# Kernel optimization log

Measured on AMD Instinct MI355X. Metric: run time of the kernel, lower is better.

The kernel has to match this reference:

```python
import jax, jax.numpy as jnp
import numpy as np

EPS = 1e-5

def _bn_train(x, gamma, beta):
    # BatchNorm2d in training mode: batch stats over (N,H,W), biased variance
    mean = jnp.mean(x, axis=(0, 2, 3), keepdims=True)
    var = jnp.mean((x - mean) ** 2, axis=(0, 2, 3), keepdims=True)
    xn = (x - mean) / jnp.sqrt(var + EPS)
    return xn * gamma[None, :, None, None] + beta[None, :, None, None]

def _bin_act(x):
    # forward: sign(x); backward: grad of clamp(x,-1,1) (STE)
    c = jnp.clip(x, -1.0, 1.0)
    return jax.lax.stop_gradient(jnp.sign(x) - c) + c

def _bin_conv(x, w_flat, out_chn, in_chn, k=3, stride=1, padding=1):
    w = w_flat.reshape(out_chn, in_chn, k, k)
    scale = jax.lax.stop_gradient(jnp.mean(jnp.abs(w), axis=(1, 2, 3), keepdims=True))
    cw = jnp.clip(w, -1.0, 1.0)
    bw = jax.lax.stop_gradient(scale * jnp.sign(w) - cw) + cw
    return jax.lax.conv_general_dilated(
        x, bw, window_strides=(stride, stride),
        padding=[(padding, padding), (padding, padding)],
        dimension_numbers=('NCHW', 'OIHW', 'NCHW'))

def _prelu(x, a):
    return jnp.where(x >= 0, x, a * x)

def setup_inputs() -> dict:
    key = jax.random.key(0)
    ks = jax.random.split(key, 4)
    C = 128
    x = jax.random.normal(ks[0], (64, C, 56, 56), dtype=jnp.float32)
    # HardBinaryConv stores weights as (n,1); init small, mixed-sign
    w1 = (jax.random.uniform(ks[1], (C * C * 9, 1), dtype=jnp.float32) - 0.5) * 0.002
    w2 = (jax.random.uniform(ks[2], (C * C * 9, 1), dtype=jnp.float32) - 0.5) * 0.002
    ones = jnp.ones((C,), jnp.float32)
    zeros = jnp.zeros((C,), jnp.float32)
    a = jnp.float32(0.25)
    return {
        'x': x,
        'bn1_g': ones, 'bn1_b': zeros,
        'w1': w1, 'prelu1_a': a,
        'bn2_g': ones, 'bn2_b': zeros,
        'w2': w2, 'prelu2_a': a,
        'bn3_g': ones, 'bn3_b': zeros,
        'prelu3_a': a,
    }

def reference(x, bn1_g, bn1_b, w1, prelu1_a, bn2_g, bn2_b, w2, prelu2_a, bn3_g, bn3_b, prelu3_a):
    C = x.shape[1]
    out = _bn_train(x, bn1_g, bn1_b)
    out = _bin_act(out)
    out = _prelu(_bin_conv(out, w1, C, C), prelu1_a)
    out = _bn_train(out, bn2_g, bn2_b)
    out = _bin_act(out)
    out = _bin_conv(out, w2, C, C)
    out = _prelu(out, prelu2_a)
    out = _bn_train(out, bn3_g, bn3_b)
    out = out + x  # identity shortcut (stride=1, in_planes==planes)
    out = _prelu(out, prelu3_a)
    return out
```

## Files before the change

### kernel.cpp

```cpp
#include <hip/hip_runtime.h>
#include <hip/hip_bf16.h>

typedef __attribute__((ext_vector_type(8))) short short8;
typedef __attribute__((ext_vector_type(4))) int i32x4;

#define HW     3136
#define M_TOT  200704
#define NTAP   9
#define NBLK   896
#define SLABB  44544

__device__ __forceinline__ void gload_lds16(const void* g, void* l) {
    __builtin_amdgcn_global_load_lds(
        (const __attribute__((address_space(1))) void*)g,
        (__attribute__((address_space(3))) void*)l, 16, 0, 0);
}

__global__ __launch_bounds__(256) void wprep_kernel(const float* __restrict__ w1,
                                                    const float* __restrict__ w2,
                                                    float* __restrict__ scale1,
                                                    float* __restrict__ scale2,
                                                    char* __restrict__ ws1,
                                                    char* __restrict__ ws2) {
    int t = threadIdx.x;
    if (blockIdx.x < 256) {
        int o = blockIdx.x;
        const float* w = w1;
        float* scale = scale1;
        if (o >= 128) { o -= 128; w = w2; scale = scale2; }
        float s = 0.f;
        for (int i = t; i < 1152; i += 256) s += fabsf(w[o * 1152 + i]);
        __shared__ float r1[256];
        r1[t] = s; __syncthreads();
        for (int off = 128; off > 0; off >>= 1) {
            if (t < off) r1[t] += r1[t + off];
            __syncthreads();
        }
        if (t == 0) scale[o] = r1[0] * (1.f / 1152.f);
        return;
    }
    int i = (blockIdx.x - 256) * 256 + t;
    const float* w = w1;
    char* wsz = ws1;
    if (i >= 147456) { i -= 147456; w = w2; wsz = ws2; }
    int e = i & 15, l = (i >> 4) & 63, f = (i >> 10) & 7, s = i >> 13;
    int cout = f * 16 + (l & 15);
    int k = s * 64 + (l >> 4) * 16 + e;
    int tap = k >> 7, cin = k & 127;
    float v = w[(cout * 128 + cin) * 9 + tap];
    wsz[i] = v > 0.f ? (char)1 : (v < 0.f ? (char)-1 : (char)0);
}

__global__ __launch_bounds__(256) void stats_nchw_kernel(const float* __restrict__ x,
                                                         float* __restrict__ psum,
                                                         float* __restrict__ psq) {
    int bid = blockIdx.x;
    int n = bid >> 7, c = bid & 127;
    const float* p = x + (n * 128 + c) * HW;
    int t = threadIdx.x;
    float s = 0.f, q = 0.f;
    for (int i4 = t; i4 < 784; i4 += 256) {
        float4 v = *(const float4*)(p + i4 * 4);
        s += v.x + v.y + v.z + v.w;
        q += v.x * v.x + v.y * v.y + v.z * v.z + v.w * v.w;
    }
    __shared__ float r1[256], r2[256];
    r1[t] = s; r2[t] = q; __syncthreads();
    for (int off = 128; off > 0; off >>= 1) {
        if (t < off) { r1[t] += r1[t + off]; r2[t] += r2[t + off]; }
        __syncthreads();
    }
    if (t == 0) { psum[c * 64 + n] = r1[0]; psq[c * 64 + n] = r2[0]; }
}

__global__ __launch_bounds__(256) void finalizeB_kernel(const float* __restrict__ psumB,
                                                        const float* __restrict__ psqB,
                                                        float* __restrict__ mean,
                                                        float* __restrict__ rstd) {
    int c = blockIdx.x, t = threadIdx.x;
    float s = 0.f, q = 0.f;
    for (int j = t; j < NBLK; j += 256) { s += psumB[j * 128 + c]; q += psqB[j * 128 + c]; }
    __shared__ float r1[256], r2[256];
    r1[t] = s; r2[t] = q; __syncthreads();
    for (int off = 128; off > 0; off >>= 1) {
        if (t < off) { r1[t] += r1[t + off]; r2[t] += r2[t + off]; }
        __syncthreads();
    }
    if (t == 0) {
        const float invN = 1.f / 200704.f;
        float m = r1[0] * invN;
        float var = r2[0] * invN - m * m;
        mean[c] = m;
        rstd[c] = 1.f / sqrtf(var + 1e-5f);
    }
}

__global__ __launch_bounds__(256) void act1_kernel(const float* __restrict__ x,
        const float* __restrict__ psum, const float* __restrict__ psq,
        const float* __restrict__ g, const float* __restrict__ b,
        char* __restrict__ apad) {
    __shared__ float row[128 * 57];
    __shared__ float smean[128], srstd[128];
    int blk = blockIdx.x;
    int n = blk / 58, hp = blk - n * 58;
    char* o = apad + (n * 58 + hp) * 58 * 128;
    int t = threadIdx.x;
    if (hp == 0 || hp == 57) {
        for (int i4 = t; i4 < 58 * 32; i4 += 256)
            *(char4*)(o + i4 * 4) = make_char4(0, 0, 0, 0);
        return;
    }
    if (t < 128) {
        float s = 0.f, q = 0.f;
        for (int j = 0; j < 64; ++j) { s += psum[t * 64 + j]; q += psq[t * 64 + j]; }
        const float invN = 1.f / 200704.f;
        float m = s * invN;
        float var = q * invN - m * m;
        smean[t] = m;
        srstd[t] = 1.f / sqrtf(var + 1e-5f);
    }
    const float* src = x + n * (128 * HW) + (hp - 1) * 56;
    for (int i4 = t; i4 < 128 * 14; i4 += 256) {
        int c = i4 / 14, w4 = (i4 - c * 14) * 4;
        float4 v = *(const float4*)(src + c * HW + w4);
        row[c * 57 + w4 + 0] = v.x;
        row[c * 57 + w4 + 1] = v.y;
        row[c * 57 + w4 + 2] = v.z;
        row[c * 57 + w4 + 3] = v.w;
    }
    __syncthreads();
    for (int i4 = t; i4 < 58 * 32; i4 += 256) {
        int wp = i4 >> 5;
        int c0 = (i4 & 31) * 4;
        char q[4] = {0, 0, 0, 0};
        if (wp >= 1 && wp <= 56) {
#pragma unroll
            for (int k = 0; k < 4; ++k) {
                int c = c0 + k;
                float xn = (row[c * 57 + wp - 1] - smean[c]) * srstd[c] * g[c] + b[c];
                q[k] = xn > 0.f ? 1 : (xn < 0.f ? -1 : 0);
            }
        }
        *(char4*)(o + wp * 128 + c0) = make_char4(q[0], q[1], q[2], q[3]);
    }
}

__global__ __launch_bounds__(256) void act2_kernel(const short* __restrict__ p1,
        const float* __restrict__ scale1, const float* __restrict__ a1ptr,
        const float* __restrict__ mean, const float* __restrict__ rstd,
        const float* __restrict__ g, const float* __restrict__ b,
        char* __restrict__ apad) {
    __shared__ float row[128 * 57];
    int blk = blockIdx.x;
    int n = blk / 58, hp = blk - n * 58;
    char* o = apad + (n * 58 + hp) * 58 * 128;
    int t = threadIdx.x;
    if (hp == 0 || hp == 57) {
        for (int i4 = t; i4 < 58 * 32; i4 += 256)
            *(char4*)(o + i4 * 4) = make_char4(0, 0, 0, 0);
        return;
    }
    float a1 = a1ptr[0];
    const short* src = p1 + n * HW + (hp - 1) * 56;
    for (int i8 = t; i8 < 128 * 7; i8 += 256) {
        int c = i8 / 7, w8 = (i8 - c * 7) * 8;
        short8 v = *(const short8*)(src + (size_t)c * M_TOT + w8);
        float sc = scale1[c];
#pragma unroll
        for (int k = 0; k < 8; ++k) {
            float val = sc * (float)v[k];
            row[c * 57 + w8 + k] = val >= 0.f ? val : a1 * val;
        }
    }
    __syncthreads();
    for (int i4 = t; i4 < 58 * 32; i4 += 256) {
        int wp = i4 >> 5;
        int c0 = (i4 & 31) * 4;
        char q[4] = {0, 0, 0, 0};
        if (wp >= 1 && wp <= 56) {
#pragma unroll
            for (int k = 0; k < 4; ++k) {
                int c = c0 + k;
                float xn = (row[c * 57 + wp - 1] - mean[c]) * rstd[c] * g[c] + b[c];
                q[k] = xn > 0.f ? 1 : (xn < 0.f ? -1 : 0);
            }
        }
        *(char4*)(o + wp * 128 + c0) = make_char4(q[0], q[1], q[2], q[3]);
    }
}

template<bool RAW, typename OutT>
__global__ __launch_bounds__(256, 2) void conv_kernel(
        const char* __restrict__ apad,
        const char* __restrict__ wswz,
        const float* __restrict__ scale,
        const float* __restrict__ aptr,
        OutT* __restrict__ obuf,
        float* __restrict__ psumB,
        float* __restrict__ psqB) {
    __shared__ __align__(1024) char lds[SLABB + 2 * 16384];

    const int tid = threadIdx.x;
    const int lane = tid & 63;
    const int wid = tid >> 6;
    const int l15 = lane & 15;
    const int lq = lane >> 4;
    const int wr = wid >> 1;
    const int wc = wid & 1;

    int bid = blockIdx.x;
    int mblk = (bid & 7) * 112 + (bid >> 3);
    const int n = mblk / 14;
    const int hg = mblk - n * 14;
    const int m0 = n * HW + hg * 224;

    const char* slabsrc = apad + (size_t)(n * 58 + hg * 4) * 58 * 128;
    char* slab = lds;
    char* Abuf = lds + SLABB;

    {
#pragma unroll
        for (int i = 0; i < 11; ++i) {
            int gbyte = i * 4096 + tid * 16;
            if (i < 10 || gbyte < SLABB) {
                int r = gbyte >> 7;
                int cp = (gbyte >> 4) & 7;
                int wp = r % 58;
                gload_lds16(slabsrc + (gbyte & ~127) + ((cp ^ (wp & 7)) << 4),
                            slab + i * 4096 + wid * 1024);
            }
        }
    }

    int Pm[7], Wm[7];
#pragma unroll
    for (int mi = 0; mi < 7; ++mi) {
        int mloc = wc * 112 + mi * 16 + l15;
        int ho = mloc / 56;
        int w = mloc - ho * 56;
        Pm[mi] = (ho * 58 + w) * 128;
        Wm[mi] = w;
    }

    auto stageA = [&](int t, int buf) {
        const char* wsrc = wswz + t * 16384 + tid * 16;
        char* dst = Abuf + buf * 16384 + wid * 1024;
#pragma unroll
        for (int i = 0; i < 4; ++i)
            gload_lds16(wsrc + i * 4096, dst + i * 4096);
    };

    i32x4 acc[4][7];
#pragma unroll
    for (int i = 0; i < 4; ++i)
#pragma unroll
        for (int j = 0; j < 7; ++j)
            acc[i][j] = (i32x4){0, 0, 0, 0};

    stageA(0, 0);

    for (int t = 0; t < NTAP; ++t) {
        asm volatile("s_waitcnt vmcnt(0)" ::: "memory");
        __builtin_amdgcn_s_barrier();
        if (t + 1 < NTAP) stageA(t + 1, (t + 1) & 1);

        int dh = t / 3;
        int dw = t - dh * 3;
        int Q = (dh * 58 + dw) * 128;
        const char* abuf = Abuf + (t & 1) * 16384;

#pragma unroll
        for (int ks = 0; ks < 2; ++ks) {
            i32x4 af[4], bf[7];
#pragma unroll
            for (int ci = 0; ci < 4; ++ci)
                af[ci] = *(const i32x4*)(abuf + ks * 8192 + (wr * 4 + ci) * 1024 + lane * 16);
            int c16 = ks * 4 + lq;
#pragma unroll
            for (int mi = 0; mi < 7; ++mi) {
                int wxd = (Wm[mi] + dw) & 7;
                bf[mi] = *(const i32x4*)(slab + Pm[mi] + Q + ((c16 ^ wxd) << 4));
            }
            __builtin_amdgcn_s_setprio(1);
#pragma unroll
            for (int ci = 0; ci < 4; ++ci)
#pragma unroll
                for (int mi = 0; mi < 7; ++mi)
                    acc[ci][mi] = __builtin_amdgcn_mfma_i32_16x16x64_i8(
                        af[ci], bf[mi], acc[ci][mi], 0, 0, 0);
            __builtin_amdgcn_s_setprio(0);
        }
    }

    float alpha = aptr[0];
    float* partS = (float*)(Abuf + 16384);
    float* partQ = (float*)(Abuf + 16384 + 1024);
#pragma unroll
    for (int ci = 0; ci < 4; ++ci) {
        int cb = wr * 64 + ci * 16 + lq * 4;
#pragma unroll
        for (int r = 0; r < 4; ++r) {
            float sc = scale[cb + r];
            OutT* op = obuf + (size_t)(cb + r) * M_TOT + m0 + wc * 112 + l15;
            float s = 0.f, q = 0.f;
#pragma unroll
            for (int mi = 0; mi < 7; ++mi) {
                int iv = acc[ci][mi][r];
                float v = (float)iv * sc;
                float pv = v >= 0.f ? v : alpha * v;
                if constexpr (RAW) op[mi * 16] = (OutT)(short)iv;
                else               op[mi * 16] = (OutT)__float2bfloat16(pv);
                s += pv; q += pv * pv;
            }
#pragma unroll
            for (int msk = 1; msk <= 8; msk <<= 1) {
                s += __shfl_xor(s, msk, 64);
                q += __shfl_xor(q, msk, 64);
            }
            if (l15 == 0) { partS[wc * 128 + cb + r] = s; partQ[wc * 128 + cb + r] = q; }
        }
    }
    __syncthreads();
    if (tid < 128) {
        psumB[bid * 128 + tid] = partS[tid] + partS[128 + tid];
        psqB [bid * 128 + tid] = partQ[tid] + partQ[128 + tid];
    }
}

__global__ __launch_bounds__(256) void final_kernel(const __hip_bfloat16* __restrict__ p2,
        const float* __restrict__ x,
        const float* __restrict__ mean, const float* __restrict__ rstd,
        const float* __restrict__ g, const float* __restrict__ b,
        const float* __restrict__ a3ptr, float* __restrict__ out) {
    int bid = blockIdx.x;
    int n = bid >> 7, c = bid & 127;
    float m = mean[c], r = rstd[c], gg = g[c], bb = b[c], a3 = a3ptr[0];
    const __hip_bfloat16* pp = p2 + (size_t)c * M_TOT + n * HW;
    const float* xx = x + (n * 128 + c) * HW;
    float* oo = out + (n * 128 + c) * HW;
    int t = threadIdx.x;
    for (int i8 = t; i8 < 392; i8 += 256) {
        short8 v = *(const short8*)(pp + i8 * 8);
        float4 x0 = *(const float4*)(xx + i8 * 8);
        float4 x1 = *(const float4*)(xx + i8 * 8 + 4);
        float o[8];
#pragma unroll
        for (int k = 0; k < 8; ++k) {
            float pv = __uint_as_float(((unsigned int)(unsigned short)v[k]) << 16);
            float xv = (k < 4) ? ((const float*)&x0)[k] : ((const float*)&x1)[k - 4];
            float val = (pv - m) * r * gg + bb + xv;
            o[k] = val >= 0.f ? val : a3 * val;
        }
        *(float4*)(oo + i8 * 8)     = make_float4(o[0], o[1], o[2], o[3]);
        *(float4*)(oo + i8 * 8 + 4) = make_float4(o[4], o[5], o[6], o[7]);
    }
}

extern "C" void kernel_launch(void* const* d_in, const int* in_sizes, int n_in,
                              void* d_out, int out_size, void* d_ws, size_t ws_size,
                              hipStream_t stream) {
    const float* x  = (const float*)d_in[0];
    const float* g1 = (const float*)d_in[1];
    const float* b1 = (const float*)d_in[2];
    const float* w1 = (const float*)d_in[3];
    const float* a1 = (const float*)d_in[4];
    const float* g2 = (const float*)d_in[5];
    const float* b2 = (const float*)d_in[6];
    const float* w2 = (const float*)d_in[7];
    const float* a2 = (const float*)d_in[8];
    const float* g3 = (const float*)d_in[9];
    const float* b3 = (const float*)d_in[10];
    const float* a3 = (const float*)d_in[11];
    float* out = (float*)d_out;
    char* ws = (char*)d_ws;

    float* scale1 = (float*)(ws);
    float* scale2 = (float*)(ws + 512);
    float* mean2  = (float*)(ws + 2048);
    float* rstd2  = (float*)(ws + 2560);
    float* mean3  = (float*)(ws + 3072);
    float* rstd3  = (float*)(ws + 3584);
    float* psum   = (float*)(ws + 4096);
    float* psq    = (float*)(ws + 36864);
    float* psumB  = (float*)(ws + 69632);
    float* psqB   = (float*)(ws + 872448);
    char* wswz1   = (char*)(ws + 1675264);
    char* wswz2   = (char*)(ws + 1822720);
    char* apad8   = (char*)(ws + 1970176);
    __hip_bfloat16* buf2b = (__hip_bfloat16*)(ws + 29528064);
    short* buf1s  = (short*)out;

    wprep_kernel<<<1408, 256, 0, stream>>>(w1, w2, scale1, scale2, wswz1, wswz2);

    stats_nchw_kernel<<<8192, 256, 0, stream>>>(x, psum, psq);
    act1_kernel<<<3712, 256, 0, stream>>>(x, psum, psq, g1, b1, apad8);
    conv_kernel<true, short><<<NBLK, 256, 0, stream>>>(apad8, wswz1, scale1, a1,
                                                       buf1s, psumB, psqB);

    finalizeB_kernel<<<128, 256, 0, stream>>>(psumB, psqB, mean2, rstd2);
    act2_kernel<<<3712, 256, 0, stream>>>(buf1s, scale1, a1, mean2, rstd2, g2, b2, apad8);
    conv_kernel<false, __hip_bfloat16><<<NBLK, 256, 0, stream>>>(apad8, wswz2, scale2, a2,
                                                                 buf2b, psumB, psqB);

    finalizeB_kernel<<<128, 256, 0, stream>>>(psumB, psqB, mean3, rstd3);
    final_kernel<<<8192, 256, 0, stream>>>(buf2b, x, mean3, rstd3, g3, b3, a3, out);
}
```

Baseline: 242.7 us.

## Shrink weight LDS staging to single half-tap buffer for 3 blocks/CU

Removes the double-buffered 16KB-per-tap weight staging and instead loads an 8KB half-tap chunk each of 18 steps into a single buffer. The smaller LDS footprint (about 54KB instead of 76KB) and launch bounds raised to 3 blocks per CU aim to increase occupancy. The cost is that weight loads are no longer prefetched: each step waits on its own global load and adds a second barrier, so latency hiding now depends on the extra resident blocks. Accumulator register pressure under the tighter launch bound may also cause spills.

```diff
diff --git a/kernel.cpp b/kernel.cpp
--- a/kernel.cpp
+++ b/kernel.cpp
@@ -6,7 +6,7 @@
 
 #define HW     3136
 #define M_TOT  200704
-#define NTAP   9
+#define NSTEP  18
 #define NBLK   896
 #define SLABB  44544
 
@@ -190,7 +190,7 @@
 }
 
 template<bool RAW, typename OutT>
-__global__ __launch_bounds__(256, 2) void conv_kernel(
+__global__ __launch_bounds__(256, 3) void conv_kernel(
         const char* __restrict__ apad,
         const char* __restrict__ wswz,
         const float* __restrict__ scale,
@@ -198,7 +198,7 @@
         OutT* __restrict__ obuf,
         float* __restrict__ psumB,
         float* __restrict__ psqB) {
-    __shared__ __align__(1024) char lds[SLABB + 2 * 16384];
+    __shared__ __align__(1024) char lds[SLABB + 8192 + 2048];
 
     const int tid = threadIdx.x;
     const int lane = tid & 63;
@@ -242,14 +242,6 @@
         Wm[mi] = w;
     }
 
-    auto stageA = [&](int t, int buf) {
-        const char* wsrc = wswz + t * 16384 + tid * 16;
-        char* dst = Abuf + buf * 16384 + wid * 1024;
-#pragma unroll
-        for (int i = 0; i < 4; ++i)
-            gload_lds16(wsrc + i * 4096, dst + i * 4096);
-    };
-
     i32x4 acc[4][7];
 #pragma unroll
     for (int i = 0; i < 4; ++i)
@@ -257,44 +249,42 @@
         for (int j = 0; j < 7; ++j)
             acc[i][j] = (i32x4){0, 0, 0, 0};
 
-    stageA(0, 0);
-
-    for (int t = 0; t < NTAP; ++t) {
+    for (int s = 0; s < NSTEP; ++s) {
+        const char* wsrc = wswz + s * 8192 + tid * 16;
+        gload_lds16(wsrc,        Abuf + wid * 1024);
+        gload_lds16(wsrc + 4096, Abuf + 4096 + wid * 1024);
         asm volatile("s_waitcnt vmcnt(0)" ::: "memory");
         __builtin_amdgcn_s_barrier();
-        if (t + 1 < NTAP) stageA(t + 1, (t + 1) & 1);
-
-        int dh = t / 3;
-        int dw = t - dh * 3;
+
+        int tap = s >> 1;
+        int dh = tap / 3;
+        int dw = tap - dh * 3;
         int Q = (dh * 58 + dw) * 128;
-        const char* abuf = Abuf + (t & 1) * 16384;
-
-#pragma unroll
-        for (int ks = 0; ks < 2; ++ks) {
-            i32x4 af[4], bf[7];
-#pragma unroll
-            for (int ci = 0; ci < 4; ++ci)
-                af[ci] = *(const i32x4*)(abuf + ks * 8192 + (wr * 4 + ci) * 1024 + lane * 16);
-            int c16 = ks * 4 + lq;
-#pragma unroll
-            for (int mi = 0; mi < 7; ++mi) {
-                int wxd = (Wm[mi] + dw) & 7;
-                bf[mi] = *(const i32x4*)(slab + Pm[mi] + Q + ((c16 ^ wxd) << 4));
-            }
-            __builtin_amdgcn_s_setprio(1);
-#pragma unroll
-            for (int ci = 0; ci < 4; ++ci)
-#pragma unroll
-                for (int mi = 0; mi < 7; ++mi)
-                    acc[ci][mi] = __builtin_amdgcn_mfma_i32_16x16x64_i8(
-                        af[ci], bf[mi], acc[ci][mi], 0, 0, 0);
-            __builtin_amdgcn_s_setprio(0);
-        }
+        int c16 = (s & 1) * 4 + lq;
+
+        i32x4 af[4], bf[7];
+#pragma unroll
+        for (int ci = 0; ci < 4; ++ci)
+            af[ci] = *(const i32x4*)(Abuf + (wr * 4 + ci) * 1024 + lane * 16);
+#pragma unroll
+        for (int mi = 0; mi < 7; ++mi) {
+            int wxd = (Wm[mi] + dw) & 7;
+            bf[mi] = *(const i32x4*)(slab + Pm[mi] + Q + ((c16 ^ wxd) << 4));
+        }
+        __builtin_amdgcn_s_setprio(1);
+#pragma unroll
+        for (int ci = 0; ci < 4; ++ci)
+#pragma unroll
+            for (int mi = 0; mi < 7; ++mi)
+                acc[ci][mi] = __builtin_amdgcn_mfma_i32_16x16x64_i8(
+                    af[ci], bf[mi], acc[ci][mi], 0, 0, 0);
+        __builtin_amdgcn_s_setprio(0);
+        __builtin_amdgcn_s_barrier();
     }
 
     float alpha = aptr[0];
-    float* partS = (float*)(Abuf + 16384);
-    float* partQ = (float*)(Abuf + 16384 + 1024);
+    float* partS = (float*)(lds + SLABB + 8192);
+    float* partQ = (float*)(lds + SLABB + 8192 + 1024);
 #pragma unroll
     for (int ci = 0; ci < 4; ++ci) {
         int cb = wr * 64 + ci * 16 + lq * 4;
```

Measured after the change: 295.4 us. 1.22x slower.
